# Kernel tuning notes

Hardware: AMD Instinct MI355X
Metric: run time of the kernel (lower is better)

The kernel has to match this reference:

```python
import jax, jax.numpy as jnp
import numpy as np

BATCH = 131072
FEAS = 256
K = 256
DEPTH = 3


def setup_inputs() -> dict:
    key = jax.random.key(0)
    ks = jax.random.split(key, 16)
    # deep tower dims: k//1 -> k//2 -> k//3 -> k//4  == 256 -> 128 -> 85 -> 64
    dims = [K // i for i in range(1, DEPTH + 2)]
    inp = {
        "x": jax.random.normal(ks[0], (BATCH, FEAS), jnp.float32),
        "w_wide": jax.random.normal(ks[1], (FEAS, 1), jnp.float32) * 0.02,
        "b_wide": jnp.zeros((1,), jnp.float32),
        # nn.Parameter(torch.rand(feas, k)) -> uniform [0,1)
        "V": jax.random.uniform(ks[2], (FEAS, K), jnp.float32),
    }
    for i in range(DEPTH):
        fan_in, fan_out = dims[i], dims[i + 1]
        inp[f"w{i+1}"] = jax.random.normal(ks[3 + 2 * i], (fan_in, fan_out), jnp.float32) * (1.0 / np.sqrt(fan_in))
        inp[f"b{i+1}"] = jnp.zeros((fan_out,), jnp.float32)
    inp["w_out"] = jax.random.normal(ks[12], (dims[-1], 1), jnp.float32) * (1.0 / np.sqrt(dims[-1]))
    inp["b_out"] = jnp.zeros((1,), jnp.float32)
    return inp


def reference(x, w_wide, b_wide, V, w1, b1, w2, b2, w3, b3, w_out, b_out):
    # wide (linear) part: [B, 1]
    linear = x @ w_wide + b_wide
    # FM bi-interaction pooling. Original loop: sum_{j >= i} x_i x_j (v_i * v_j)
    # (break/continue on zeros only skip zero-valued terms). Including the
    # diagonal, this equals 0.5 * ((x @ V)^2 + (x^2) @ (V^2)).  [B, K]
    xv = x @ V
    x2v2 = (x * x) @ (V * V)
    tmp = 0.5 * (xv * xv + x2v2)
    # deep tower: Linear + ReLU at each depth
    for w, b in ((w1, b1), (w2, b2), (w3, b3)):
        tmp = jax.nn.relu(tmp @ w + b)
    deep_out = tmp @ w_out + b_out  # [B, 1]
    return jax.nn.sigmoid(linear + deep_out)
```

## Files before the change

kernel.cpp:

```cpp
#include <hip/hip_runtime.h>
#include <math.h>


typedef _Float16 f16;
typedef _Float16 f16x4 __attribute__((ext_vector_type(4)));
typedef _Float16 f16x8 __attribute__((ext_vector_type(8)));
typedef float f32x4 __attribute__((ext_vector_type(4)));

#define NROWS   131072
#define ROWS    64
#define FDIM    256
#define KDIM    256
#define D1      128
#define D2      85
#define D2P     96

#define SSTRIDE 136

#define OFF_VT_H   0x0UL
#define OFF_VT_L   0x20000UL
#define OFF_V2T    0x40000UL
#define OFF_W1T_H  0x60000UL
#define OFF_W1T_L  0x70000UL
#define OFF_W2T_H  0x80000UL
#define OFF_W2T_L  0x86000UL
#define OFF_W3T_H  0x8C000UL
#define OFF_W3T_L  0x8F000UL

static __device__ __forceinline__ f32x4 mfma16(f16x8 a, f16x8 b, f32x4 c) {
  return __builtin_amdgcn_mfma_f32_16x16x32_f16(a, b, c, 0, 0, 0);
}

__global__ __launch_bounds__(256) void prep_kernel(
    const float* __restrict__ V, const float* __restrict__ w1,
    const float* __restrict__ w2, const float* __restrict__ w3,
    f16* VT_h, f16* VT_l, f16* V2T,
    f16* W1T_h, f16* W1T_l, f16* W2T_h, f16* W2T_l, f16* W3T_h, f16* W3T_l) {
  int idx0 = blockIdx.x * 256 + threadIdx.x;
  int stride = gridDim.x * 256;
  for (int idx = idx0; idx < KDIM * FDIM; idx += stride) {
    int k = idx >> 8, i = idx & 255;
    float v = V[i * KDIM + k];
    f16 h = (f16)v;
    VT_h[idx] = h;
    VT_l[idx] = (f16)(v - (float)h);
    V2T[idx] = (f16)(v * v);
  }
  for (int idx = idx0; idx < D1 * KDIM; idx += stride) {
    int n = idx >> 8, k = idx & 255;
    float w = w1[k * D1 + n];
    f16 h = (f16)w;
    W1T_h[idx] = h;
    W1T_l[idx] = (f16)(w - (float)h);
  }
  for (int idx = idx0; idx < D2P * D1; idx += stride) {
    int n = idx >> 7, k = idx & 127;
    float w = (n < D2) ? w2[k * D2 + n] : 0.f;
    f16 h = (f16)w;
    W2T_h[idx] = h;
    W2T_l[idx] = (f16)(w - (float)h);
  }
  for (int idx = idx0; idx < 64 * D2P; idx += stride) {
    int n = idx / D2P, k = idx - n * D2P;
    float w = (k < D2) ? w3[k * 64 + n] : 0.f;
    f16 h = (f16)w;
    W3T_h[idx] = h;
    W3T_l[idx] = (f16)(w - (float)h);
  }
}

__global__ __launch_bounds__(512, 4) void fused_kernel(
    const float* __restrict__ x, const float* __restrict__ w_wide,
    const float* __restrict__ b_wide,
    const f16* __restrict__ VT_h, const f16* __restrict__ VT_l,
    const f16* __restrict__ V2T,
    const f16* __restrict__ W1T_h, const f16* __restrict__ W1T_l,
    const float* __restrict__ b1,
    const f16* __restrict__ W2T_h, const f16* __restrict__ W2T_l,
    const float* __restrict__ b2,
    const f16* __restrict__ W3T_h, const f16* __restrict__ W3T_l,
    const float* __restrict__ b3,
    const float* __restrict__ w_out, const float* __restrict__ b_out,
    float* __restrict__ out) {
  __shared__ __align__(16) f16 smem[32768];
  __shared__ float linS[ROWS];
  __shared__ float pfS[ROWS * 2];

  f16* sXh  = smem;
  f16* sXl  = smem + 8704;
  f16* sX2  = smem + 17408;
  f16* tmpH = smem;
  f16* tmpL = smem + 16384;
  f16* h1H  = smem + 16384;
  f16* h1L  = smem + 24576;
  f16* h2H  = smem;
  f16* h2L  = smem + 8192;

  const int tid = threadIdx.x;
  const int lane = tid & 63, wv = tid >> 6;
  const int q = lane >> 4, ln = lane & 15;
  const int row0 = blockIdx.x * ROWS;
  const int sr = tid >> 3, sc = (tid & 7) * 16;

  f32x4 accV[4][2], acc2[4][2];
#pragma unroll
  for (int i = 0; i < 4; ++i)
#pragma unroll
    for (int j = 0; j < 2; ++j) {
      accV[i][j] = (f32x4){0.f, 0.f, 0.f, 0.f};
      acc2[i][j] = (f32x4){0.f, 0.f, 0.f, 0.f};
    }
  float linp = 0.f;

  for (int kk = 0; kk < 2; ++kk) {
    const int kbase = kk * 128;
    float4 a[4], w4[4];
    const float* xp = x + (size_t)(row0 + sr) * FDIM + kbase + sc;
    const float* wp = w_wide + kbase + sc;
#pragma unroll
    for (int t = 0; t < 4; ++t) {
      a[t] = *(const float4*)(xp + t * 4);
      w4[t] = *(const float4*)(wp + t * 4);
    }
    __syncthreads();
#pragma unroll
    for (int t = 0; t < 4; ++t) {
      linp += a[t].x * w4[t].x + a[t].y * w4[t].y + a[t].z * w4[t].z +
              a[t].w * w4[t].w;
      float f0[4] = {a[t].x, a[t].y, a[t].z, a[t].w};
      f16x4 h0, l0, q0;
#pragma unroll
      for (int j = 0; j < 4; ++j) {
        f16 h = (f16)f0[j];
        h0[j] = h;
        l0[j] = (f16)(f0[j] - (float)h);
        q0[j] = (f16)(f0[j] * f0[j]);
      }
      int off0 = sr * SSTRIDE + sc + t * 4;
      *(f16x4*)(sXh + off0) = h0;
      *(f16x4*)(sXl + off0) = l0;
      *(f16x4*)(sX2 + off0) = q0;
    }
    __syncthreads();

#pragma unroll
    for (int ks = 0; ks < 4; ++ks) {
      const int k0 = kbase + ks * 32;
      f16x8 Bh[2], Bl[2], B2[2];
#pragma unroll
      for (int ni = 0; ni < 2; ++ni) {
        int n = wv * 32 + ni * 16 + ln;
        size_t boff = (size_t)n * FDIM + k0 + q * 8;
        Bh[ni] = *(const f16x8*)(VT_h + boff);
        Bl[ni] = *(const f16x8*)(VT_l + boff);
        B2[ni] = *(const f16x8*)(V2T + boff);
      }
#pragma unroll
      for (int mi = 0; mi < 4; ++mi) {
        int aoff = (mi * 16 + ln) * SSTRIDE + ks * 32 + q * 8;
        f16x8 Ah = *(const f16x8*)(sXh + aoff);
        f16x8 Al = *(const f16x8*)(sXl + aoff);
        f16x8 A2 = *(const f16x8*)(sX2 + aoff);
#pragma unroll
        for (int ni = 0; ni < 2; ++ni) {
          accV[mi][ni] = mfma16(Al, Bh[ni], accV[mi][ni]);
          accV[mi][ni] = mfma16(Ah, Bl[ni], accV[mi][ni]);
          accV[mi][ni] = mfma16(Ah, Bh[ni], accV[mi][ni]);
          acc2[mi][ni] = mfma16(A2, B2[ni], acc2[mi][ni]);
        }
      }
    }
  }

  {
    float s0 = linp;
    s0 += __shfl_xor(s0, 1);
    s0 += __shfl_xor(s0, 2);
    s0 += __shfl_xor(s0, 4);
    if ((tid & 7) == 0) linS[sr] = s0 + b_wide[0];
  }

  __syncthreads();

#pragma unroll
  for (int mi = 0; mi < 4; ++mi)
#pragma unroll
    for (int r = 0; r < 4; ++r) {
      int m = mi * 16 + q * 4 + r;
      int mrow = m * 256, msw = m & 7;
#pragma unroll
      for (int ni = 0; ni < 2; ++ni) {
        int n = wv * 32 + ni * 16 + ln;
        float xv = accV[mi][ni][r];
        float val = 0.5f * (xv * xv + acc2[mi][ni][r]);
        f16 hi = (f16)val;
        f16 lo = (f16)(val - (float)hi);
        int off = mrow + (((n >> 3) ^ msw) << 3) + (n & 7);
        tmpH[off] = hi;
        tmpL[off] = lo;
      }
    }

  __syncthreads();

  f32x4 acc1[4];
#pragma unroll
  for (int i = 0; i < 4; ++i) acc1[i] = (f32x4){0.f, 0.f, 0.f, 0.f};

#pragma unroll
  for (int ks = 0; ks < 8; ++ks) {
    size_t boff = (size_t)(wv * 16 + ln) * KDIM + ks * 32 + q * 8;
    f16x8 Bh = *(const f16x8*)(W1T_h + boff);
    f16x8 Bl = *(const f16x8*)(W1T_l + boff);
#pragma unroll
    for (int mi = 0; mi < 4; ++mi) {
      int m = mi * 16 + ln;
      int aoff = m * 256 + (((ks * 4 + q) ^ (m & 7)) << 3);
      f16x8 Ah = *(const f16x8*)(tmpH + aoff);
      f16x8 Al = *(const f16x8*)(tmpL + aoff);
      acc1[mi] = mfma16(Al, Bh, acc1[mi]);
      acc1[mi] = mfma16(Ah, Bl, acc1[mi]);
      acc1[mi] = mfma16(Ah, Bh, acc1[mi]);
    }
  }

  __syncthreads();

  {
    int n = wv * 16 + ln;
    float bias = b1[n];
#pragma unroll
    for (int mi = 0; mi < 4; ++mi)
#pragma unroll
      for (int r = 0; r < 4; ++r) {
        int m = mi * 16 + q * 4 + r;
        float z = acc1[mi][r] + bias;
        z = z > 0.f ? z : 0.f;
        f16 hi = (f16)z;
        f16 lo = (f16)(z - (float)hi);
        int off = m * 128 + (((n >> 3) ^ (m & 7)) << 3) + (n & 7);
        h1H[off] = hi;
        h1L[off] = lo;
      }
  }

  __syncthreads();

  const int mt = wv & 3, half = wv >> 2;
  f32x4 accL2[3];
#pragma unroll
  for (int j = 0; j < 3; ++j) accL2[j] = (f32x4){0.f, 0.f, 0.f, 0.f};

#pragma unroll
  for (int ks = 0; ks < 4; ++ks) {
    int m = mt * 16 + ln;
    int aoff = m * 128 + (((ks * 4 + q) ^ (m & 7)) << 3);
    f16x8 Ah = *(const f16x8*)(h1H + aoff);
    f16x8 Al = *(const f16x8*)(h1L + aoff);
#pragma unroll
    for (int nj = 0; nj < 3; ++nj) {
      int n = (half * 3 + nj) * 16 + ln;
      size_t boff = (size_t)n * D1 + ks * 32 + q * 8;
      f16x8 Bh = *(const f16x8*)(W2T_h + boff);
      f16x8 Bl = *(const f16x8*)(W2T_l + boff);
      accL2[nj] = mfma16(Al, Bh, accL2[nj]);
      accL2[nj] = mfma16(Ah, Bl, accL2[nj]);
      accL2[nj] = mfma16(Ah, Bh, accL2[nj]);
    }
  }

#pragma unroll
  for (int r = 0; r < 4; ++r) {
    int m = mt * 16 + q * 4 + r;
    int mrow = m * 128, msw = m & 7;
#pragma unroll
    for (int nj = 0; nj < 3; ++nj) {
      int n = (half * 3 + nj) * 16 + ln;
      float z = accL2[nj][r] + ((n < D2) ? b2[n] : 0.f);
      z = z > 0.f ? z : 0.f;
      f16 hi = (f16)z;
      f16 lo = (f16)(z - (float)hi);
      int off = mrow + (((n >> 3) ^ msw) << 3) + (n & 7);
      h2H[off] = hi;
      h2L[off] = lo;
    }
  }

  __syncthreads();

  f32x4 accL3[2];
  accL3[0] = (f32x4){0.f, 0.f, 0.f, 0.f};
  accL3[1] = (f32x4){0.f, 0.f, 0.f, 0.f};

#pragma unroll
  for (int ks = 0; ks < 3; ++ks) {
    int m = mt * 16 + ln;
    int aoff = m * 128 + (((ks * 4 + q) ^ (m & 7)) << 3);
    f16x8 Ah = *(const f16x8*)(h2H + aoff);
    f16x8 Al = *(const f16x8*)(h2L + aoff);
#pragma unroll
    for (int nj = 0; nj < 2; ++nj) {
      int n = (half * 2 + nj) * 16 + ln;
      size_t boff = (size_t)n * D2P + ks * 32 + q * 8;
      f16x8 Bh = *(const f16x8*)(W3T_h + boff);
      f16x8 Bl = *(const f16x8*)(W3T_l + boff);
      accL3[nj] = mfma16(Al, Bh, accL3[nj]);
      accL3[nj] = mfma16(Ah, Bl, accL3[nj]);
      accL3[nj] = mfma16(Ah, Bh, accL3[nj]);
    }
  }

  {
    float b3v[2], wov[2];
#pragma unroll
    for (int nj = 0; nj < 2; ++nj) {
      int n = (half * 2 + nj) * 16 + ln;
      b3v[nj] = b3[n];
      wov[nj] = w_out[n];
    }
#pragma unroll
    for (int r = 0; r < 4; ++r) {
      float part = 0.f;
#pragma unroll
      for (int nj = 0; nj < 2; ++nj) {
        float z = accL3[nj][r] + b3v[nj];
        part += (z > 0.f ? z : 0.f) * wov[nj];
      }
      part += __shfl_xor(part, 1);
      part += __shfl_xor(part, 2);
      part += __shfl_xor(part, 4);
      part += __shfl_xor(part, 8);
      if (ln == 0) pfS[(mt * 16 + q * 4 + r) * 2 + half] = part;
    }
  }

  __syncthreads();

  if (tid < ROWS) {
    float zf = linS[tid] + pfS[tid * 2] + pfS[tid * 2 + 1] + b_out[0];
    out[row0 + tid] = 1.f / (1.f + expf(-zf));
  }
}

extern "C" void kernel_launch(void* const* d_in, const int* in_sizes, int n_in,
                              void* d_out, int out_size, void* d_ws, size_t ws_size,
                              hipStream_t stream) {
  const float* x = (const float*)d_in[0];
  const float* w_wide = (const float*)d_in[1];
  const float* b_wide = (const float*)d_in[2];
  const float* V = (const float*)d_in[3];
  const float* w1 = (const float*)d_in[4];
  const float* b1 = (const float*)d_in[5];
  const float* w2 = (const float*)d_in[6];
  const float* b2 = (const float*)d_in[7];
  const float* w3 = (const float*)d_in[8];
  const float* b3 = (const float*)d_in[9];
  const float* w_out = (const float*)d_in[10];
  const float* b_out = (const float*)d_in[11];
  float* out = (float*)d_out;
  char* ws = (char*)d_ws;

  f16* VT_h = (f16*)(ws + OFF_VT_H);
  f16* VT_l = (f16*)(ws + OFF_VT_L);
  f16* V2T = (f16*)(ws + OFF_V2T);
  f16* W1T_h = (f16*)(ws + OFF_W1T_H);
  f16* W1T_l = (f16*)(ws + OFF_W1T_L);
  f16* W2T_h = (f16*)(ws + OFF_W2T_H);
  f16* W2T_l = (f16*)(ws + OFF_W2T_L);
  f16* W3T_h = (f16*)(ws + OFF_W3T_H);
  f16* W3T_l = (f16*)(ws + OFF_W3T_L);

  prep_kernel<<<64, 256, 0, stream>>>(V, w1, w2, w3, VT_h, VT_l, V2T, W1T_h,
                                      W1T_l, W2T_h, W2T_l, W3T_h, W3T_l);

  fused_kernel<<<NROWS / ROWS, 512, 0, stream>>>(
      x, w_wide, b_wide, VT_h, VT_l, V2T, W1T_h, W1T_l, b1, W2T_h, W2T_l, b2,
      W3T_h, W3T_l, b3, w_out, b_out, out);
}
```

Before: 397.9 us.

## Halve block to 32 rows and 4 waves, remap MFMA tiles, add setprio

Shrinks each block from 64 rows and 8 waves to 32 rows and 4 waves, halving shared memory per block. Each wave now covers more N columns, so the first two GEMM stages are re-tiled, with A fragments from LDS loaded once and reused across several global B fragments. s_setprio is wrapped around the MFMA groups so the scheduler favours matrix issue. The aim is more blocks per CU and better latency hiding. The cost is that each block re-reads the same weight fragments from global/L2 for only half as many rows, which doubles total weight traffic.

```diff
diff --git a/kernel.cpp b/kernel.cpp
--- a/kernel.cpp
+++ b/kernel.cpp
@@ -8,7 +8,7 @@
 typedef float f32x4 __attribute__((ext_vector_type(4)));
 
 #define NROWS   131072
-#define ROWS    64
+#define ROWS    32
 #define FDIM    256
 #define KDIM    256
 #define D1      128
@@ -69,7 +69,7 @@
   }
 }
 
-__global__ __launch_bounds__(512, 4) void fused_kernel(
+__global__ __launch_bounds__(256, 4) void fused_kernel(
     const float* __restrict__ x, const float* __restrict__ w_wide,
     const float* __restrict__ b_wide,
     const f16* __restrict__ VT_h, const f16* __restrict__ VT_l,
@@ -82,19 +82,19 @@
     const float* __restrict__ b3,
     const float* __restrict__ w_out, const float* __restrict__ b_out,
     float* __restrict__ out) {
-  __shared__ __align__(16) f16 smem[32768];
+  __shared__ __align__(16) f16 smem[16384];
   __shared__ float linS[ROWS];
   __shared__ float pfS[ROWS * 2];
 
   f16* sXh  = smem;
-  f16* sXl  = smem + 8704;
-  f16* sX2  = smem + 17408;
+  f16* sXl  = smem + 4352;
+  f16* sX2  = smem + 8704;
   f16* tmpH = smem;
-  f16* tmpL = smem + 16384;
-  f16* h1H  = smem + 16384;
-  f16* h1L  = smem + 24576;
+  f16* tmpL = smem + 8192;
+  f16* h1H  = smem + 8192;
+  f16* h1L  = smem + 12288;
   f16* h2H  = smem;
-  f16* h2L  = smem + 8192;
+  f16* h2L  = smem + 4096;
 
   const int tid = threadIdx.x;
   const int lane = tid & 63, wv = tid >> 6;
@@ -102,11 +102,11 @@
   const int row0 = blockIdx.x * ROWS;
   const int sr = tid >> 3, sc = (tid & 7) * 16;
 
-  f32x4 accV[4][2], acc2[4][2];
-#pragma unroll
-  for (int i = 0; i < 4; ++i)
-#pragma unroll
-    for (int j = 0; j < 2; ++j) {
+  f32x4 accV[2][4], acc2[2][4];
+#pragma unroll
+  for (int i = 0; i < 2; ++i)
+#pragma unroll
+    for (int j = 0; j < 4; ++j) {
       accV[i][j] = (f32x4){0.f, 0.f, 0.f, 0.f};
       acc2[i][j] = (f32x4){0.f, 0.f, 0.f, 0.f};
     }
@@ -146,28 +146,30 @@
 #pragma unroll
     for (int ks = 0; ks < 4; ++ks) {
       const int k0 = kbase + ks * 32;
-      f16x8 Bh[2], Bl[2], B2[2];
-#pragma unroll
-      for (int ni = 0; ni < 2; ++ni) {
-        int n = wv * 32 + ni * 16 + ln;
+      f16x8 Ah[2], Al[2], A2[2];
+#pragma unroll
+      for (int mi = 0; mi < 2; ++mi) {
+        int aoff = (mi * 16 + ln) * SSTRIDE + ks * 32 + q * 8;
+        Ah[mi] = *(const f16x8*)(sXh + aoff);
+        Al[mi] = *(const f16x8*)(sXl + aoff);
+        A2[mi] = *(const f16x8*)(sX2 + aoff);
+      }
+#pragma unroll
+      for (int ni = 0; ni < 4; ++ni) {
+        int n = wv * 64 + ni * 16 + ln;
         size_t boff = (size_t)n * FDIM + k0 + q * 8;
-        Bh[ni] = *(const f16x8*)(VT_h + boff);
-        Bl[ni] = *(const f16x8*)(VT_l + boff);
-        B2[ni] = *(const f16x8*)(V2T + boff);
-      }
-#pragma unroll
-      for (int mi = 0; mi < 4; ++mi) {
-        int aoff = (mi * 16 + ln) * SSTRIDE + ks * 32 + q * 8;
-        f16x8 Ah = *(const f16x8*)(sXh + aoff);
-        f16x8 Al = *(const f16x8*)(sXl + aoff);
-        f16x8 A2 = *(const f16x8*)(sX2 + aoff);
-#pragma unroll
-        for (int ni = 0; ni < 2; ++ni) {
-          accV[mi][ni] = mfma16(Al, Bh[ni], accV[mi][ni]);
-          accV[mi][ni] = mfma16(Ah, Bl[ni], accV[mi][ni]);
-          accV[mi][ni] = mfma16(Ah, Bh[ni], accV[mi][ni]);
-          acc2[mi][ni] = mfma16(A2, B2[ni], acc2[mi][ni]);
+        f16x8 Bh = *(const f16x8*)(VT_h + boff);
+        f16x8 Bl = *(const f16x8*)(VT_l + boff);
+        f16x8 B2 = *(const f16x8*)(V2T + boff);
+        __builtin_amdgcn_s_setprio(1);
+#pragma unroll
+        for (int mi = 0; mi < 2; ++mi) {
+          accV[mi][ni] = mfma16(Al[mi], Bh, accV[mi][ni]);
+          accV[mi][ni] = mfma16(Ah[mi], Bl, accV[mi][ni]);
+          accV[mi][ni] = mfma16(Ah[mi], Bh, accV[mi][ni]);
+          acc2[mi][ni] = mfma16(A2[mi], B2, acc2[mi][ni]);
         }
+        __builtin_amdgcn_s_setprio(0);
       }
     }
   }
@@ -183,14 +185,14 @@
   __syncthreads();
 
 #pragma unroll
-  for (int mi = 0; mi < 4; ++mi)
+  for (int mi = 0; mi < 2; ++mi)
 #pragma unroll
     for (int r = 0; r < 4; ++r) {
       int m = mi * 16 + q * 4 + r;
       int mrow = m * 256, msw = m & 7;
 #pragma unroll
-      for (int ni = 0; ni < 2; ++ni) {
-        int n = wv * 32 + ni * 16 + ln;
+      for (int ni = 0; ni < 4; ++ni) {
+        int n = wv * 64 + ni * 16 + ln;
         float xv = accV[mi][ni][r];
         float val = 0.5f * (xv * xv + acc2[mi][ni][r]);
         f16 hi = (f16)val;
@@ -203,38 +205,50 @@
 
   __syncthreads();
 
-  f32x4 acc1[4];
-#pragma unroll
-  for (int i = 0; i < 4; ++i) acc1[i] = (f32x4){0.f, 0.f, 0.f, 0.f};
+  f32x4 acc1[2][2];
+#pragma unroll
+  for (int i = 0; i < 2; ++i)
+#pragma unroll
+    for (int j = 0; j < 2; ++j) acc1[i][j] = (f32x4){0.f, 0.f, 0.f, 0.f};
 
 #pragma unroll
   for (int ks = 0; ks < 8; ++ks) {
-    size_t boff = (size_t)(wv * 16 + ln) * KDIM + ks * 32 + q * 8;
-    f16x8 Bh = *(const f16x8*)(W1T_h + boff);
-    f16x8 Bl = *(const f16x8*)(W1T_l + boff);
-#pragma unroll
-    for (int mi = 0; mi < 4; ++mi) {
+    f16x8 Ah[2], Al[2];
+#pragma unroll
+    for (int mi = 0; mi < 2; ++mi) {
       int m = mi * 16 + ln;
       int aoff = m * 256 + (((ks * 4 + q) ^ (m & 7)) << 3);
-      f16x8 Ah = *(const f16x8*)(tmpH + aoff);
-      f16x8 Al = *(const f16x8*)(tmpL + aoff);
-      acc1[mi] = mfma16(Al, Bh, acc1[mi]);
-      acc1[mi] = mfma16(Ah, Bl, acc1[mi]);
-      acc1[mi] = mfma16(Ah, Bh, acc1[mi]);
-    }
-  }
-
-  __syncthreads();
-
-  {
-    int n = wv * 16 + ln;
+      Ah[mi] = *(const f16x8*)(tmpH + aoff);
+      Al[mi] = *(const f16x8*)(tmpL + aoff);
+    }
+#pragma unroll
+    for (int nt = 0; nt < 2; ++nt) {
+      size_t boff = (size_t)((wv * 2 + nt) * 16 + ln) * KDIM + ks * 32 + q * 8;
+      f16x8 Bh = *(const f16x8*)(W1T_h + boff);
+      f16x8 Bl = *(const f16x8*)(W1T_l + boff);
+      __builtin_amdgcn_s_setprio(1);
+#pragma unroll
+      for (int mi = 0; mi < 2; ++mi) {
+        acc1[mi][nt] = mfma16(Al[mi], Bh, acc1[mi][nt]);
+        acc1[mi][nt] = mfma16(Ah[mi], Bl, acc1[mi][nt]);
+        acc1[mi][nt] = mfma16(Ah[mi], Bh, acc1[mi][nt]);
+      }
+      __builtin_amdgcn_s_setprio(0);
+    }
+  }
+
+  __syncthreads();
+
+#pragma unroll
+  for (int nt = 0; nt < 2; ++nt) {
+    int n = (wv * 2 + nt) * 16 + ln;
     float bias = b1[n];
 #pragma unroll
-    for (int mi = 0; mi < 4; ++mi)
+    for (int mi = 0; mi < 2; ++mi)
 #pragma unroll
       for (int r = 0; r < 4; ++r) {
         int m = mi * 16 + q * 4 + r;
-        float z = acc1[mi][r] + bias;
+        float z = acc1[mi][nt][r] + bias;
         z = z > 0.f ? z : 0.f;
         f16 hi = (f16)z;
         f16 lo = (f16)(z - (float)hi);
@@ -246,7 +260,7 @@
 
   __syncthreads();
 
-  const int mt = wv & 3, half = wv >> 2;
+  const int mt = wv & 1, half = wv >> 1;
   f32x4 accL2[3];
 #pragma unroll
   for (int j = 0; j < 3; ++j) accL2[j] = (f32x4){0.f, 0.f, 0.f, 0.f};
@@ -263,9 +277,11 @@
       size_t boff = (size_t)n * D1 + ks * 32 + q * 8;
       f16x8 Bh = *(const f16x8*)(W2T_h + boff);
       f16x8 Bl = *(const f16x8*)(W2T_l + boff);
+      __builtin_amdgcn_s_setprio(1);
       accL2[nj] = mfma16(Al, Bh, accL2[nj]);
       accL2[nj] = mfma16(Ah, Bl, accL2[nj]);
       accL2[nj] = mfma16(Ah, Bh, accL2[nj]);
+      __builtin_amdgcn_s_setprio(0);
     }
   }
 
@@ -304,9 +320,11 @@
       size_t boff = (size_t)n * D2P + ks * 32 + q * 8;
       f16x8 Bh = *(const f16x8*)(W3T_h + boff);
       f16x8 Bl = *(const f16x8*)(W3T_l + boff);
+      __builtin_amdgcn_s_setprio(1);
       accL3[nj] = mfma16(Al, Bh, accL3[nj]);
       accL3[nj] = mfma16(Ah, Bl, accL3[nj]);
       accL3[nj] = mfma16(Ah, Bh, accL3[nj]);
+      __builtin_amdgcn_s_setprio(0);
     }
   }
 
@@ -373,7 +391,7 @@
   prep_kernel<<<64, 256, 0, stream>>>(V, w1, w2, w3, VT_h, VT_l, V2T, W1T_h,
                                       W1T_l, W2T_h, W2T_l, W3T_h, W3T_l);
 
-  fused_kernel<<<NROWS / ROWS, 512, 0, stream>>>(
+  fused_kernel<<<NROWS / ROWS, 256, 0, stream>>>(
       x, w_wide, b_wide, VT_h, VT_l, V2T, W1T_h, W1T_l, b1, W2T_h, W2T_l, b2,
       W3T_h, W3T_l, b3, w_out, b_out, out);
 }
```

New measurement: 522.3 us. 31.2% more time.
